# Kernel tuning notes

Hardware: AMD Instinct MI355X
Metric: run time of the kernel (lower is better)

Reference implementation:

```python
import jax, jax.numpy as jnp
import numpy as np

DECAY = 0.99
EPS = 1e-5

def setup_inputs() -> dict:
    key = jax.random.key(0)
    k1, k2 = jax.random.split(key)
    B, D, H, W, K = 64, 256, 32, 32, 1024
    z = jax.random.normal(k1, (B, D, H, W), dtype=jnp.float32)
    embedding = jax.random.normal(k2, (K, D), dtype=jnp.float32) * 0.1
    cluster_size = jnp.zeros((K,), dtype=jnp.float32)
    embedding_avg = embedding.copy()
    return {"z": z, "embedding": embedding, "cluster_size": cluster_size,
            "embedding_avg": embedding_avg}

def reference(z, embedding, cluster_size, embedding_avg):
    B, D, H, W = z.shape
    K = embedding.shape[0]
    # [B,D,H,W] -> [N,D], N = B*H*W
    flat_z = jnp.transpose(z, (0, 2, 3, 1)).reshape(-1, D)
    # squared L2 distances to codebook: [N,K]
    distances = (jnp.sum(flat_z * flat_z, axis=1, keepdims=True)
                 + jnp.sum(embedding * embedding, axis=1)
                 - 2.0 * jnp.matmul(flat_z, embedding.T))
    encoding_indices = jnp.argmin(distances, axis=1)          # [N]
    quantized = embedding[encoding_indices]                    # [N,D] (gather == one-hot matmul)
    quantized = jnp.transpose(quantized.reshape(B, H, W, D), (0, 3, 1, 2))
    # per-code statistics (== encodings.sum(0) and encodings.T @ flat_z)
    counts = jax.ops.segment_sum(jnp.ones((flat_z.shape[0],), dtype=flat_z.dtype),
                                 encoding_indices, num_segments=K)  # [K]
    embed_sum = jax.ops.segment_sum(flat_z, encoding_indices, num_segments=K)  # [K,D]
    # EMA buffer updates (training path)
    cluster_size_new = DECAY * cluster_size + (1.0 - DECAY) * counts
    embedding_avg_new = DECAY * embedding_avg + (1.0 - DECAY) * embed_sum
    n = jnp.sum(cluster_size_new)
    smoothed = (cluster_size_new + EPS) / (n + K * EPS) * n
    embedding_new = embedding_avg_new / smoothed[:, None]
    # straight-through quantization
    z_q = z + jax.lax.stop_gradient(quantized - z)
    loss = jnp.mean(jnp.square(jax.lax.stop_gradient(z_q) - z))
    indices = encoding_indices.reshape(B, H, W)
    avg_probs = counts / counts.sum()
    perplexity = jnp.exp(-jnp.sum(avg_probs * jnp.log(avg_probs + 1e-10)))
    used_codes = (counts > 0).astype(flat_z.dtype)
    return (z_q, loss, indices, perplexity, used_codes,
            embedding_new, cluster_size_new, embedding_avg_new)
```

## Files before the change

kernel.cpp:

```cpp
#include <hip/hip_runtime.h>
#include <hip/hip_bf16.h>

#define D_   256
#define K_   1024
#define HW_  1024
#define B_   64
#define N_   65536

#define OFF_ZQ   ((size_t)0)
#define OFF_LOSS ((size_t)16777216)
#define OFF_IDX  ((size_t)16777217)
#define OFF_PERP ((size_t)16842753)
#define OFF_USED ((size_t)16842754)
#define OFF_ENEW ((size_t)16843778)
#define OFF_CSN  ((size_t)17105922)
#define OFF_EAVG ((size_t)17106946)

#define DECAY_F 0.99f
#define W_NEW   ((float)(1.0 - 0.99))
#define EPS_F   1e-5f
#define KEPS_F  ((float)(1024.0 * 1e-5))
#define MARGIN  0.00390625f

#define WS_E2      0
#define WS_CNT     1024
#define WS_LOSS    2048
#define WS_FLAGCNT 2052
#define WS_SMOO    2304
#define WS_OFFS    3328
#define WS_CURS    4352
#define WS_Z2      8192
#define WS_BUCKET  73728
#define WS_FLAG    139264

typedef __attribute__((ext_vector_type(8))) short bf16x8;
typedef __attribute__((ext_vector_type(8))) unsigned short u16x8;
typedef __attribute__((ext_vector_type(4))) float f32x4;

static __device__ __forceinline__ float bf2f(unsigned short u) {
    return __uint_as_float(((unsigned int)u) << 16);
}
static __device__ __forceinline__ unsigned short f2bf(float x) {
    unsigned int u = __float_as_uint(x);
    return (unsigned short)((u + 0x7fffu + ((u >> 16) & 1u)) >> 16);
}

__global__ __launch_bounds__(256) void prep_z(
    const float* __restrict__ z, unsigned short* __restrict__ zhi,
    unsigned short* __restrict__ zlo, float* __restrict__ z2g) {
    __shared__ float tile[128][68];
    __shared__ double zred[64][4];
    const int tid = threadIdx.x;
    const int b   = blockIdx.x >> 4;
    const int hw0 = (blockIdx.x & 15) * 64;
    const float* zb = z + (size_t)b * (D_ * HW_);

    const int hw = tid >> 2, dq = tid & 3;
    double zacc = 0.0;

    for (int h = 0; h < 2; ++h) {
        #pragma unroll
        for (int ch = 0; ch < 8; ++ch) {
            int d = h * 128 + ch * 16 + (tid >> 4);
            int c4 = (tid & 15) * 4;
            float4 v = *(const float4*)&zb[(size_t)d * HW_ + hw0 + c4];
            tile[ch * 16 + (tid >> 4)][c4 + 0] = v.x;
            tile[ch * 16 + (tid >> 4)][c4 + 1] = v.y;
            tile[ch * 16 + (tid >> 4)][c4 + 2] = v.z;
            tile[ch * 16 + (tid >> 4)][c4 + 3] = v.w;
        }
        __syncthreads();
        size_t pt = (size_t)b * HW_ + hw0 + hw;
        #pragma unroll
        for (int jb = 0; jb < 4; ++jb) {
            unsigned short hs[8], ls[8];
            #pragma unroll
            for (int e = 0; e < 8; ++e) {
                float v = tile[dq * 32 + jb * 8 + e][hw];
                zacc += (double)v * (double)v;
                unsigned short hh = f2bf(v);
                hs[e] = hh;
                ls[e] = f2bf(v - bf2f(hh));
            }
            size_t dst = pt * D_ + h * 128 + dq * 32 + jb * 8;
            *(u16x8*)&zhi[dst] = *(u16x8*)hs;
            *(u16x8*)&zlo[dst] = *(u16x8*)ls;
        }
        __syncthreads();
    }
    zred[hw][dq] = zacc;
    __syncthreads();
    if (tid < 64) {
        double s = zred[tid][0] + zred[tid][1] + zred[tid][2] + zred[tid][3];
        z2g[b * HW_ + hw0 + tid] = (float)s;
    }
}

__global__ __launch_bounds__(64) void prep_e(
    const float* __restrict__ E, unsigned short* __restrict__ ehi,
    unsigned short* __restrict__ elo, float* __restrict__ e2g) {
    int k = blockIdx.x;
    int lane = threadIdx.x;
    float4 v = *(const float4*)&E[(size_t)k * D_ + lane * 4];
    double s = (double)v.x * v.x + (double)v.y * v.y +
               (double)v.z * v.z + (double)v.w * v.w;
    float vv[4] = {v.x, v.y, v.z, v.w};
    ushort4 hs, ls;
    unsigned short* hp = (unsigned short*)&hs;
    unsigned short* lp = (unsigned short*)&ls;
    #pragma unroll
    for (int e = 0; e < 4; ++e) {
        unsigned short hh = f2bf(vv[e]);
        hp[e] = hh;
        lp[e] = f2bf(vv[e] - bf2f(hh));
    }
    *(ushort4*)&ehi[(size_t)k * D_ + lane * 4] = hs;
    *(ushort4*)&elo[(size_t)k * D_ + lane * 4] = ls;
    #pragma unroll
    for (int m = 32; m > 0; m >>= 1) s += __shfl_xor(s, m, 64);
    if (lane == 0) e2g[k] = (float)s;
}

__global__ __launch_bounds__(256) void argmin_mfma(
    const unsigned short* __restrict__ zhi, const unsigned short* __restrict__ zlo,
    const unsigned short* __restrict__ ehi, const unsigned short* __restrict__ elo,
    const float* __restrict__ e2g, float* __restrict__ out_idx,
    int* __restrict__ flagged, int* __restrict__ flagcnt) {
    __shared__ unsigned short zl[2][128][40];
    __shared__ float mred[2][128][3];

    const int tid  = threadIdx.x;
    const int lane = tid & 63;
    const int wid  = tid >> 6;
    const int wr = wid >> 1, wc = wid & 1;
    const int x = lane & 15, g = lane >> 4;
    const int pt0 = blockIdx.x * 128;

    const int spt = tid & 127;
    const int spl = tid >> 7;
    const unsigned short* zsrc = (spl ? zlo : zhi) + (size_t)(pt0 + spt) * D_;

    float m1[16], m2[16];
    int   a1[16];
    #pragma unroll
    for (int s = 0; s < 16; ++s) { m1[s] = 3.4e38f; m2[s] = 3.4e38f; a1[s] = 0; }

    for (int kt = 0; kt < 8; ++kt) {
        f32x4 acc[4][4];
        #pragma unroll
        for (int mf = 0; mf < 4; ++mf)
            #pragma unroll
            for (int nf = 0; nf < 4; ++nf) acc[mf][nf] = (f32x4)0.f;

        for (int dc = 0; dc < 8; ++dc) {
            u16x8 s0 = *(const u16x8*)&zsrc[dc * 32 + 0];
            u16x8 s1 = *(const u16x8*)&zsrc[dc * 32 + 8];
            u16x8 s2 = *(const u16x8*)&zsrc[dc * 32 + 16];
            u16x8 s3 = *(const u16x8*)&zsrc[dc * 32 + 24];
            __syncthreads();
            *(u16x8*)&zl[spl][spt][0]  = s0;
            *(u16x8*)&zl[spl][spt][8]  = s1;
            *(u16x8*)&zl[spl][spt][16] = s2;
            *(u16x8*)&zl[spl][spt][24] = s3;
            __syncthreads();

            bf16x8 bh[4], bl[4];
            #pragma unroll
            for (int nf = 0; nf < 4; ++nf) {
                int code = kt * 128 + wc * 64 + nf * 16 + x;
                size_t base = (size_t)code * D_ + dc * 32 + g * 8;
                bh[nf] = *(const bf16x8*)&ehi[base];
                bl[nf] = *(const bf16x8*)&elo[base];
            }
            bf16x8 ah[4], al[4];
            #pragma unroll
            for (int mf = 0; mf < 4; ++mf) {
                int pt = wr * 64 + mf * 16 + x;
                ah[mf] = *(const bf16x8*)&zl[0][pt][g * 8];
                al[mf] = *(const bf16x8*)&zl[1][pt][g * 8];
            }
            #pragma unroll
            for (int mf = 0; mf < 4; ++mf)
                #pragma unroll
                for (int nf = 0; nf < 4; ++nf) {
                    acc[mf][nf] = __builtin_amdgcn_mfma_f32_16x16x32_bf16(ah[mf], bh[nf], acc[mf][nf], 0, 0, 0);
                    acc[mf][nf] = __builtin_amdgcn_mfma_f32_16x16x32_bf16(ah[mf], bl[nf], acc[mf][nf], 0, 0, 0);
                    acc[mf][nf] = __builtin_amdgcn_mfma_f32_16x16x32_bf16(al[mf], bh[nf], acc[mf][nf], 0, 0, 0);
                }
        }

        float e2v[4];
        int   cbase[4];
        #pragma unroll
        for (int nf = 0; nf < 4; ++nf) {
            cbase[nf] = kt * 128 + wc * 64 + nf * 16 + x;
            e2v[nf] = e2g[cbase[nf]];
        }
        #pragma unroll
        for (int mf = 0; mf < 4; ++mf)
            #pragma unroll
            for (int reg = 0; reg < 4; ++reg) {
                int s = mf * 4 + reg;
                #pragma unroll
                for (int nf = 0; nf < 4; ++nf) {
                    float dist = __builtin_fmaf(-2.0f, acc[mf][nf][reg], e2v[nf]);
                    if (dist < m1[s]) { m2[s] = m1[s]; m1[s] = dist; a1[s] = cbase[nf]; }
                    else m2[s] = fminf(m2[s], dist);
                }
            }
    }

    #pragma unroll
    for (int mask = 1; mask < 16; mask <<= 1) {
        #pragma unroll
        for (int s = 0; s < 16; ++s) {
            float om1 = __shfl_xor(m1[s], mask, 64);
            int   oa  = __shfl_xor(a1[s], mask, 64);
            float om2 = __shfl_xor(m2[s], mask, 64);
            bool take = (om1 < m1[s]) || (om1 == m1[s] && oa < a1[s]);
            float loser = take ? m1[s] : om1;
            m2[s] = fminf(fminf(m2[s], om2), loser);
            if (take) { m1[s] = om1; a1[s] = oa; }
        }
    }
    if (x < 4) {
        #pragma unroll
        for (int reg = 0; reg < 4; ++reg) {
            int s = x * 4 + reg;
            int ptl = wr * 64 + x * 16 + g * 4 + reg;
            mred[wc][ptl][0] = m1[s];
            mred[wc][ptl][1] = (float)a1[s];
            mred[wc][ptl][2] = m2[s];
        }
    }
    __syncthreads();
    if (tid < 128) {
        float am1 = mred[0][tid][0], bm1 = mred[1][tid][0];
        int   aa  = (int)mred[0][tid][1], ba = (int)mred[1][tid][1];
        float am2 = mred[0][tid][2], bm2 = mred[1][tid][2];
        bool take = (bm1 < am1) || (bm1 == am1 && ba < aa);
        float m1f = take ? bm1 : am1;
        int   a1f = take ? ba : aa;
        float m2f = fminf(fminf(am2, bm2), take ? am1 : bm1);
        out_idx[pt0 + tid] = (float)a1f;
        if (m2f - m1f < MARGIN) {
            int pos = atomicAdd(flagcnt, 1);
            flagged[pos] = pt0 + tid;
        }
    }
}

__global__ __launch_bounds__(256) void rescue_kernel(
    const float* __restrict__ z, const float* __restrict__ E,
    const float* __restrict__ e2g, const float* __restrict__ z2g,
    const int* __restrict__ flagged, const int* __restrict__ flagcnt,
    float* __restrict__ out_idx) {
    __shared__ float zs[8][257];
    __shared__ float zz[8];
    __shared__ float redm[256];
    __shared__ int   reda[256];
    const int tid = threadIdx.x;
    const int nflag = flagcnt[0];
    const int nb = (nflag + 7) >> 3;

    for (int bi = blockIdx.x; bi < nb; bi += gridDim.x) {
        int base = bi * 8;
        int cnt = nflag - base; if (cnt > 8) cnt = 8;
        for (int j = 0; j < cnt; ++j) {
            int p = flagged[base + j];
            zs[j][tid] = z[(size_t)(p >> 10) * (D_ * HW_) + (size_t)tid * HW_ + (p & 1023)];
        }
        if (tid < cnt) zz[tid] = z2g[flagged[base + tid]];
        __syncthreads();

        float mj[8], distc[8];
        int   aj[8];
        #pragma unroll
        for (int j = 0; j < 8; ++j) { mj[j] = 3.4e38f; aj[j] = 0; }

        for (int c = 0; c < 4; ++c) {
            int code = tid * 4 + c;
            const float* er = E + (size_t)code * D_;
            float accj[8];
            #pragma unroll
            for (int j = 0; j < 8; ++j) accj[j] = 0.f;
            for (int d = 0; d < D_; ++d) {
                float ev = er[d];
                #pragma unroll
                for (int j = 0; j < 8; ++j)
                    accj[j] = __builtin_fmaf(ev, zs[j][d], accj[j]);
            }
            float e2c = e2g[code];
            #pragma unroll
            for (int j = 0; j < 8; ++j) {
                distc[j] = __fsub_rn(__fadd_rn(zz[j], e2c), __fmul_rn(2.0f, accj[j]));
                if (distc[j] < mj[j]) { mj[j] = distc[j]; aj[j] = code; }
            }
        }
        for (int j = 0; j < cnt; ++j) {
            redm[tid] = mj[j]; reda[tid] = aj[j];
            __syncthreads();
            for (int s = 128; s > 0; s >>= 1) {
                if (tid < s) {
                    float om = redm[tid + s]; int oa = reda[tid + s];
                    if (om < redm[tid] || (om == redm[tid] && oa < reda[tid])) {
                        redm[tid] = om; reda[tid] = oa;
                    }
                }
                __syncthreads();
            }
            if (tid == 0) out_idx[flagged[base + j]] = (float)reda[0];
            __syncthreads();
        }
        __syncthreads();
    }
}

__global__ __launch_bounds__(256) void count_kernel(
    const float* __restrict__ idxf, float* __restrict__ counts) {
    int n = blockIdx.x * 256 + threadIdx.x;
    unsafeAtomicAdd(&counts[(int)idxf[n]], 1.0f);
}

__global__ __launch_bounds__(256) void quant_kernel(
    const float* __restrict__ z, const float* __restrict__ E,
    const float* __restrict__ idxf, float* __restrict__ zq,
    float* __restrict__ lossacc) {
    const int b  = blockIdx.x >> 4;
    const int d0 = (blockIdx.x & 15) * 16;
    const int tid = threadIdx.x;
    const int hw = tid * 4;
    const float* zb = z  + (size_t)b * (D_ * HW_);
    float*       qb = zq + (size_t)b * (D_ * HW_);

    int idx[4];
    #pragma unroll
    for (int i = 0; i < 4; ++i) idx[i] = (int)idxf[b * HW_ + hw + i];

    float loss = 0.f;
    for (int db = 0; db < 4; ++db) {
        int d = d0 + db * 4;
        float qa[4][4];
        #pragma unroll
        for (int i = 0; i < 4; ++i)
            *(float4*)&qa[i][0] = *(const float4*)&E[(size_t)idx[i] * D_ + d];
        #pragma unroll
        for (int dd = 0; dd < 4; ++dd) {
            float4 z4 = *(const float4*)&zb[(size_t)(d + dd) * HW_ + hw];
            float zv[4] = {z4.x, z4.y, z4.z, z4.w};
            float o[4];
            #pragma unroll
            for (int i = 0; i < 4; ++i) {
                float diff = __fsub_rn(qa[i][dd], zv[i]);
                float zqv  = __fadd_rn(zv[i], diff);
                o[i] = zqv;
                float l = __fsub_rn(zqv, zv[i]);
                loss = __builtin_fmaf(l, l, loss);
            }
            *(float4*)&qb[(size_t)(d + dd) * HW_ + hw] = make_float4(o[0], o[1], o[2], o[3]);
        }
    }
    __shared__ float ls[256];
    ls[tid] = loss;
    __syncthreads();
    for (int s = 128; s > 0; s >>= 1) {
        if (tid < s) ls[tid] += ls[tid + s];
        __syncthreads();
    }
    if (tid == 0) unsafeAtomicAdd(lossacc, ls[0]);
}

__global__ __launch_bounds__(1024) void fin1(
    const float* __restrict__ counts, const float* __restrict__ cs_in,
    float* __restrict__ out, float* __restrict__ smoothed) {
    const int k = threadIdx.x;
    __shared__ float red[1024];
    float c = counts[k];
    float csn = __fadd_rn(__fmul_rn(DECAY_F, cs_in[k]), __fmul_rn(W_NEW, c));
    out[OFF_CSN + k]  = csn;
    out[OFF_USED + k] = (c > 0.f) ? 1.f : 0.f;
    red[k] = csn; __syncthreads();
    for (int s = 512; s > 0; s >>= 1) { if (k < s) red[k] += red[k + s]; __syncthreads(); }
    float n_ = red[0]; __syncthreads();
    red[k] = c; __syncthreads();
    for (int s = 512; s > 0; s >>= 1) { if (k < s) red[k] += red[k + s]; __syncthreads(); }
    float total = red[0]; __syncthreads();
    float p = c / total;
    red[k] = p * logf(p + 1e-10f); __syncthreads();
    for (int s = 512; s > 0; s >>= 1) { if (k < s) red[k] += red[k + s]; __syncthreads(); }
    if (k == 0) out[OFF_PERP] = expf(-red[0]);
    smoothed[k] = __fmul_rn(__fdiv_rn(__fadd_rn(csn, EPS_F), __fadd_rn(n_, KEPS_F)), n_);
}

__global__ void fin_loss(const float* __restrict__ lossacc, float* __restrict__ out) {
    if (threadIdx.x == 0) out[OFF_LOSS] = lossacc[0] / 16777216.0f;
}

__global__ __launch_bounds__(1024) void scan_kernel(
    const float* __restrict__ counts, int* __restrict__ offs,
    int* __restrict__ cursor) {
    __shared__ int s[1024];
    const int k = threadIdx.x;
    int c = (int)counts[k];
    s[k] = c; __syncthreads();
    for (int dlt = 1; dlt < 1024; dlt <<= 1) {
        int v = (k >= dlt) ? s[k - dlt] : 0;
        __syncthreads();
        s[k] += v;
        __syncthreads();
    }
    int off = s[k] - c;
    offs[k] = off;
    cursor[k] = off;
}

__global__ __launch_bounds__(256) void scatter_kernel(
    const float* __restrict__ idxf, int* __restrict__ cursor,
    int* __restrict__ bucket) {
    int n = blockIdx.x * 256 + threadIdx.x;
    int k = (int)idxf[n];
    int pos = atomicAdd(&cursor[k], 1);
    bucket[pos] = n;
}

__global__ __launch_bounds__(256) void code_update(
    const unsigned short* __restrict__ zhi, const unsigned short* __restrict__ zlo,
    const float* __restrict__ eavg_in, const float* __restrict__ smoothed,
    const float* __restrict__ counts, const int* __restrict__ offs,
    const int* __restrict__ bucket, float* __restrict__ out) {
    const int k = blockIdx.x;
    const int d = threadIdx.x;
    const int off = offs[k];
    const int cnt = (int)counts[k];
    float acc = 0.f;
    for (int i = 0; i < cnt; ++i) {
        int p = bucket[off + i];
        size_t base = (size_t)p * D_ + d;
        acc += bf2f(zhi[base]) + bf2f(zlo[base]);
    }
    int e = k * D_ + d;
    float ean = __fadd_rn(__fmul_rn(DECAY_F, eavg_in[e]), __fmul_rn(W_NEW, acc));
    out[OFF_EAVG + e] = ean;
    out[OFF_ENEW + e] = __fdiv_rn(ean, smoothed[k]);
}

extern "C" void kernel_launch(void* const* d_in, const int* in_sizes, int n_in,
                              void* d_out, int out_size, void* d_ws, size_t ws_size,
                              hipStream_t stream) {
    const float* z    = (const float*)d_in[0];
    const float* E    = (const float*)d_in[1];
    const float* cs   = (const float*)d_in[2];
    const float* eavg = (const float*)d_in[3];
    float* out = (float*)d_out;
    float* wsf = (float*)d_ws;
    int*   wsi = (int*)d_ws;

    unsigned short* zhiP = (unsigned short*)(out + OFF_ZQ);
    unsigned short* zloP = zhiP + (size_t)N_ * D_;
    unsigned short* ehiP = (unsigned short*)(out + OFF_ENEW);
    unsigned short* eloP = ehiP + (size_t)K_ * D_;

    hipMemsetAsync(d_ws, 0, 32768, stream);

    prep_z<<<1024, 256, 0, stream>>>(z, zhiP, zloP, wsf + WS_Z2);
    prep_e<<<K_, 64, 0, stream>>>(E, ehiP, eloP, wsf + WS_E2);
    argmin_mfma<<<N_ / 128, 256, 0, stream>>>(zhiP, zloP, ehiP, eloP,
                                              wsf + WS_E2, out + OFF_IDX,
                                              wsi + WS_FLAG, wsi + WS_FLAGCNT);
    rescue_kernel<<<256, 256, 0, stream>>>(z, E, wsf + WS_E2, wsf + WS_Z2,
                                           wsi + WS_FLAG, wsi + WS_FLAGCNT,
                                           out + OFF_IDX);
    count_kernel<<<N_ / 256, 256, 0, stream>>>(out + OFF_IDX, wsf + WS_CNT);
    fin1<<<1, 1024, 0, stream>>>(wsf + WS_CNT, cs, out, wsf + WS_SMOO);
    scan_kernel<<<1, 1024, 0, stream>>>(wsf + WS_CNT, wsi + WS_OFFS, wsi + WS_CURS);
    scatter_kernel<<<N_ / 256, 256, 0, stream>>>(out + OFF_IDX, wsi + WS_CURS,
                                                 wsi + WS_BUCKET);
    code_update<<<K_, 256, 0, stream>>>(zhiP, zloP, eavg, wsf + WS_SMOO,
                                        wsf + WS_CNT, wsi + WS_OFFS,
                                        wsi + WS_BUCKET, out);
    quant_kernel<<<B_ * 16, 256, 0, stream>>>(z, E, out + OFF_IDX, out + OFF_ZQ,
                                              wsf + WS_LOSS);
    fin_loss<<<1, 64, 0, stream>>>(wsf + WS_LOSS, out);
}
```

Baseline: 656.0 us.

## Stage full 64-point z tile in swizzled LDS once, split codes across waves

The argmin kernel now loads the whole 64-point by 256-dim hi/lo z tile into XOR-swizzled shared memory once per block, instead of restaging 32-dim slices with two barriers per step. Each of the four waves now covers a different quarter of the codebook for all 64 points, and partial minima are merged across four waves at the end. The grid doubles to 1024 blocks, and launch bounds request two blocks per CU. This removes the repeated barriers and global reloads of z, but each block now reads the full codebook for only 64 points, halving codebook reuse per block, and uses 64KB of LDS per block, which may limit occupancy.

```diff
diff --git a/kernel.cpp b/kernel.cpp
--- a/kernel.cpp
+++ b/kernel.cpp
@@ -121,31 +121,40 @@
     if (lane == 0) e2g[k] = (float)s;
 }
 
-__global__ __launch_bounds__(256) void argmin_mfma(
+__global__ __launch_bounds__(256, 2) void argmin_mfma(
     const unsigned short* __restrict__ zhi, const unsigned short* __restrict__ zlo,
     const unsigned short* __restrict__ ehi, const unsigned short* __restrict__ elo,
     const float* __restrict__ e2g, float* __restrict__ out_idx,
     int* __restrict__ flagged, int* __restrict__ flagcnt) {
-    __shared__ unsigned short zl[2][128][40];
-    __shared__ float mred[2][128][3];
+    __shared__ unsigned short zl[2][64][256];
+    float (*mred)[64][3] = (float(*)[64][3])&zl[0][0][0];
 
     const int tid  = threadIdx.x;
     const int lane = tid & 63;
     const int wid  = tid >> 6;
-    const int wr = wid >> 1, wc = wid & 1;
     const int x = lane & 15, g = lane >> 4;
-    const int pt0 = blockIdx.x * 128;
-
-    const int spt = tid & 127;
-    const int spl = tid >> 7;
-    const unsigned short* zsrc = (spl ? zlo : zhi) + (size_t)(pt0 + spt) * D_;
+    const int pt0 = blockIdx.x * 64;
+
+    {
+        const unsigned short* s0 = zhi + (size_t)pt0 * D_;
+        const unsigned short* s1 = zlo + (size_t)pt0 * D_;
+        #pragma unroll
+        for (int i = 0; i < 8; ++i) {
+            int c = i * 256 + tid;
+            int pt = c >> 5, d16 = c & 31;
+            int soff = (d16 * 8) ^ ((pt & 7) << 3);
+            *(u16x8*)&zl[0][pt][soff] = *(const u16x8*)&s0[c * 8];
+            *(u16x8*)&zl[1][pt][soff] = *(const u16x8*)&s1[c * 8];
+        }
+    }
+    __syncthreads();
 
     float m1[16], m2[16];
     int   a1[16];
     #pragma unroll
     for (int s = 0; s < 16; ++s) { m1[s] = 3.4e38f; m2[s] = 3.4e38f; a1[s] = 0; }
 
-    for (int kt = 0; kt < 8; ++kt) {
+    for (int kt = 0; kt < 4; ++kt) {
         f32x4 acc[4][4];
         #pragma unroll
         for (int mf = 0; mf < 4; ++mf)
@@ -153,31 +162,21 @@
             for (int nf = 0; nf < 4; ++nf) acc[mf][nf] = (f32x4)0.f;
 
         for (int dc = 0; dc < 8; ++dc) {
-            u16x8 s0 = *(const u16x8*)&zsrc[dc * 32 + 0];
-            u16x8 s1 = *(const u16x8*)&zsrc[dc * 32 + 8];
-            u16x8 s2 = *(const u16x8*)&zsrc[dc * 32 + 16];
-            u16x8 s3 = *(const u16x8*)&zsrc[dc * 32 + 24];
-            __syncthreads();
-            *(u16x8*)&zl[spl][spt][0]  = s0;
-            *(u16x8*)&zl[spl][spt][8]  = s1;
-            *(u16x8*)&zl[spl][spt][16] = s2;
-            *(u16x8*)&zl[spl][spt][24] = s3;
-            __syncthreads();
-
+            bf16x8 ah[4], al[4];
+            #pragma unroll
+            for (int mf = 0; mf < 4; ++mf) {
+                int pt = mf * 16 + x;
+                int soff = (dc * 32 + g * 8) ^ ((pt & 7) << 3);
+                ah[mf] = *(const bf16x8*)&zl[0][pt][soff];
+                al[mf] = *(const bf16x8*)&zl[1][pt][soff];
+            }
             bf16x8 bh[4], bl[4];
             #pragma unroll
             for (int nf = 0; nf < 4; ++nf) {
-                int code = kt * 128 + wc * 64 + nf * 16 + x;
+                int code = kt * 256 + wid * 64 + nf * 16 + x;
                 size_t base = (size_t)code * D_ + dc * 32 + g * 8;
                 bh[nf] = *(const bf16x8*)&ehi[base];
                 bl[nf] = *(const bf16x8*)&elo[base];
-            }
-            bf16x8 ah[4], al[4];
-            #pragma unroll
-            for (int mf = 0; mf < 4; ++mf) {
-                int pt = wr * 64 + mf * 16 + x;
-                ah[mf] = *(const bf16x8*)&zl[0][pt][g * 8];
-                al[mf] = *(const bf16x8*)&zl[1][pt][g * 8];
             }
             #pragma unroll
             for (int mf = 0; mf < 4; ++mf)
@@ -193,7 +192,7 @@
         int   cbase[4];
         #pragma unroll
         for (int nf = 0; nf < 4; ++nf) {
-            cbase[nf] = kt * 128 + wc * 64 + nf * 16 + x;
+            cbase[nf] = kt * 256 + wid * 64 + nf * 16 + x;
             e2v[nf] = e2g[cbase[nf]];
         }
         #pragma unroll
@@ -223,25 +222,30 @@
             if (take) { m1[s] = om1; a1[s] = oa; }
         }
     }
+    __syncthreads();
     if (x < 4) {
         #pragma unroll
         for (int reg = 0; reg < 4; ++reg) {
             int s = x * 4 + reg;
-            int ptl = wr * 64 + x * 16 + g * 4 + reg;
-            mred[wc][ptl][0] = m1[s];
-            mred[wc][ptl][1] = (float)a1[s];
-            mred[wc][ptl][2] = m2[s];
+            int ptl = x * 16 + g * 4 + reg;
+            mred[wid][ptl][0] = m1[s];
+            mred[wid][ptl][1] = (float)a1[s];
+            mred[wid][ptl][2] = m2[s];
         }
     }
     __syncthreads();
-    if (tid < 128) {
-        float am1 = mred[0][tid][0], bm1 = mred[1][tid][0];
-        int   aa  = (int)mred[0][tid][1], ba = (int)mred[1][tid][1];
-        float am2 = mred[0][tid][2], bm2 = mred[1][tid][2];
-        bool take = (bm1 < am1) || (bm1 == am1 && ba < aa);
-        float m1f = take ? bm1 : am1;
-        int   a1f = take ? ba : aa;
-        float m2f = fminf(fminf(am2, bm2), take ? am1 : bm1);
+    if (tid < 64) {
+        float m1f = mred[0][tid][0], m2f = mred[0][tid][2];
+        int   a1f = (int)mred[0][tid][1];
+        #pragma unroll
+        for (int w = 1; w < 4; ++w) {
+            float om1 = mred[w][tid][0], om2 = mred[w][tid][2];
+            int   oa  = (int)mred[w][tid][1];
+            bool take = (om1 < m1f) || (om1 == m1f && oa < a1f);
+            float loser = take ? m1f : om1;
+            m2f = fminf(fminf(m2f, om2), loser);
+            if (take) { m1f = om1; a1f = oa; }
+        }
         out_idx[pt0 + tid] = (float)a1f;
         if (m2f - m1f < MARGIN) {
             int pos = atomicAdd(flagcnt, 1);
@@ -464,9 +468,9 @@
 
     prep_z<<<1024, 256, 0, stream>>>(z, zhiP, zloP, wsf + WS_Z2);
     prep_e<<<K_, 64, 0, stream>>>(E, ehiP, eloP, wsf + WS_E2);
-    argmin_mfma<<<N_ / 128, 256, 0, stream>>>(zhiP, zloP, ehiP, eloP,
-                                              wsf + WS_E2, out + OFF_IDX,
-                                              wsi + WS_FLAG, wsi + WS_FLAGCNT);
+    argmin_mfma<<<N_ / 64, 256, 0, stream>>>(zhiP, zloP, ehiP, eloP,
+                                             wsf + WS_E2, out + OFF_IDX,
+                                             wsi + WS_FLAG, wsi + WS_FLAGCNT);
     rescue_kernel<<<256, 256, 0, stream>>>(z, E, wsf + WS_E2, wsf + WS_Z2,
                                            wsi + WS_FLAG, wsi + WS_FLAGCNT,
                                            out + OFF_IDX);
```

After: 857.3 us. 30.7% more time.
